# Optimization experiments

Measured on AMD Instinct MI355X. Metric: run time of the kernel, lower is better.

## Reference

```python
import jax, jax.numpy as jnp
import numpy as np

# Dims from init_kwargs
B, L, D = 32, 512, 1024
NSEC = 4
SSIZE = D // NSEC          # 256
LATENT = 256
N_TOKENS = 32
BANDS = ((0, 64), (16, 128), (32, 192), (64, 256))
COEF = 0.1


def _dct_mat(N):
    # torch_dct.dct (DCT-II, unnormalized, factor 2): X[k] = 2*sum_n x[n] cos(pi*k*(2n+1)/(2N))
    n = jnp.arange(N, dtype=jnp.float32)
    k = jnp.arange(N, dtype=jnp.float32)[:, None]
    return 2.0 * jnp.cos(jnp.pi * (2.0 * n + 1.0) * k / (2.0 * N))  # [k, n]


def _idct_mat(N):
    # exact inverse of the above (DCT-III form): x[n] = (1/N)*(X[0]/2 + sum_{k>=1} X[k] cos(pi*k*(2n+1)/(2N)))
    k = jnp.arange(N, dtype=jnp.float32)
    n = jnp.arange(N, dtype=jnp.float32)[:, None]
    M = jnp.cos(jnp.pi * k * (2.0 * n + 1.0) / (2.0 * N)) / N
    return M.at[:, 0].set(1.0 / (2.0 * N))  # [n, k]


def setup_inputs() -> dict:
    key = jax.random.key(0)
    k1, k2, k3 = jax.random.split(key, 3)
    encoding = jax.random.normal(k1, (B, L, D), dtype=jnp.float32)
    W = jax.random.normal(k2, (LATENT, SSIZE), dtype=jnp.float32) / np.float32(np.sqrt(SSIZE))
    b = jax.random.normal(k3, (LATENT,), dtype=jnp.float32) * 0.01
    return {"encoding": encoding, "W": W, "b": b}


def reference(encoding, W, b):
    # encoding: [B, L, D] -> [B, L, NSEC, SSIZE]
    enc = encoding.reshape(B, L, NSEC, SSIZE)
    # Literal semantics of the torch code: H = enc[:,:,i] is [B,L,S]; H.T -> [S,L,B];
    # dct/idct act over the LAST axis (= batch), scaling indexes the seq axis.
    C = _dct_mat(B)   # [k, b]
    M = _idct_mat(B)  # [b, k]
    # DCT along batch axis for all sectors at once: [k, L, NSEC, SSIZE]
    Dk = jnp.einsum('kb,blns->klns', C, enc)
    # Per-sector band scaling along the seq axis
    seq = jnp.arange(L)
    mask = jnp.stack(
        [jnp.where((seq < lo) | (seq >= hi), jnp.float32(COEF), jnp.float32(1.0)) for (lo, hi) in BANDS],
        axis=1,
    )  # [L, NSEC]
    Dk = Dk * mask[None, :, :, None]
    # IDCT back along batch axis: [B, L, NSEC, SSIZE]
    filt = jnp.einsum('bk,klns->blns', M, Dk)
    # Linear(SSIZE -> LATENT) + tanh, then keep first N_TOKENS positions
    y = jnp.tanh(jnp.einsum('blns,os->blno', filt, W) + b)
    return y[:, :N_TOKENS]
```

## Files before the change

kernel.cpp:

```cpp
#include <hip/hip_runtime.h>
#include <math.h>

#define LSEQ   512
#define DDIM   1024
#define KDIM   256
#define COLS   256
#define ROWS   4096
#define COEF   0.1f

#define TR     64
#define TC     64
#define BK     128


__device__ __forceinline__ float tanh_fast(float x) {
    return 1.0f - 2.0f / (__expf(2.0f * x) + 1.0f);
}

__global__ __launch_bounds__(256, 1)
void spectral_gemm_kernel(const float* __restrict__ enc,
                          const float* __restrict__ W,
                          const float* __restrict__ bias,
                          float* __restrict__ out) {
    __shared__ float4 As[TR * (BK / 4)];
    __shared__ float4 Ws[TC * (BK / 4)];

    const int t      = threadIdx.x;
    const int tile_r = blockIdx.x * TR;
    const int tile_c = blockIdx.y * TC;

    const float4* __restrict__ srcA =
        (const float4*)(enc + (size_t)(tile_r >> 7) * (size_t)(LSEQ * DDIM)
                            + (size_t)(tile_r & 127) * KDIM);
    const float4* __restrict__ srcW = (const float4*)(W + (size_t)tile_c * KDIM);

    const int tx = t & 15, ty = t >> 4;
    const int sA = ty & 7;
    const int sW = tx & 7;
    const int ra = ty * 4;
    const int ca = tx * 4;

    float acc[4][4] = {{0.f,0.f,0.f,0.f},{0.f,0.f,0.f,0.f},
                       {0.f,0.f,0.f,0.f},{0.f,0.f,0.f,0.f}};

    for (int p = 0; p < 2; ++p) {
        if (p) __syncthreads();

        #pragma unroll
        for (int i = 0; i < 8; ++i) {
            const int f    = t + i * 256;
            const int r    = f >> 5;
            const int k4   = f & 31;
            const int phys = k4 ^ ((r >> 2) & 7);
            As[r * 32 + phys] = srcA[r * 64 + 32 * p + k4];
            Ws[r * 32 + phys] = srcW[r * 64 + 32 * p + k4];
        }
        __syncthreads();

        #pragma unroll 8
        for (int k4 = 0; k4 < 32; ++k4) {
            const int pa = k4 ^ sA;
            const int pw = k4 ^ sW;
            float4 a[4], w[4];
            #pragma unroll
            for (int i = 0; i < 4; ++i) a[i] = As[(ra + i) * 32 + pa];
            #pragma unroll
            for (int j = 0; j < 4; ++j) w[j] = Ws[(ca + j) * 32 + pw];
            #pragma unroll
            for (int i = 0; i < 4; ++i)
                #pragma unroll
                for (int j = 0; j < 4; ++j) {
                    acc[i][j] += a[i].x * w[j].x;
                    acc[i][j] += a[i].y * w[j].y;
                    acc[i][j] += a[i].z * w[j].z;
                    acc[i][j] += a[i].w * w[j].w;
                }
        }
    }

    const float4 b4 = *(const float4*)&bias[tile_c + ca];
    #pragma unroll
    for (int i = 0; i < 4; ++i) {
        const int row = tile_r + ra + i;
        const int n = row & 3;
        const int l = (row >> 2) & 31;
        const float scale = (n == 0 || (n == 1 && l >= 16)) ? 1.0f : COEF;
        float4 o;
        o.x = tanh_fast(scale * acc[i][0] + b4.x);
        o.y = tanh_fast(scale * acc[i][1] + b4.y);
        o.z = tanh_fast(scale * acc[i][2] + b4.z);
        o.w = tanh_fast(scale * acc[i][3] + b4.w);
        *(float4*)&out[(size_t)row * COLS + tile_c + ca] = o;
    }
}

extern "C" void kernel_launch(void* const* d_in, const int* in_sizes, int n_in,
                              void* d_out, int out_size, void* d_ws, size_t ws_size,
                              hipStream_t stream) {
    const float* enc  = (const float*)d_in[0];
    const float* W    = (const float*)d_in[1];
    const float* bias = (const float*)d_in[2];
    float* out = (float*)d_out;

    dim3 grid(ROWS / TR, COLS / TC);
    spectral_gemm_kernel<<<grid, dim3(256), 0, stream>>>(enc, W, bias, out);
}
```

Measured before the change: 101.1 us.

## Use split-bf16 MFMA matrix cores for the projection GEMM

Replaces the FP32 FMA inner loop with bf16 MFMA 16x16x32 instructions, splitting each fp32 value into high and low bf16 parts and using three products to approximate fp32 accuracy. Row tile is halved to 32 so the grid gets more blocks, and launch bounds now allow two blocks per CU. The goal is to cut vector ALU time on a GEMM of 4096x256x256. In exchange, the split conversion in the load path adds VALU work, and the result carries a small precision loss compared with true fp32.

Result: faster. 93.72 us (-7.3%).

```diff
diff --git a/kernel.cpp b/kernel.cpp
--- a/kernel.cpp
+++ b/kernel.cpp
@@ -8,89 +8,127 @@
 #define ROWS   4096
 #define COEF   0.1f
 
-#define TR     64
+#define TR     32
 #define TC     64
 #define BK     128
+#define RSTR   128
 
+
+typedef __attribute__((ext_vector_type(8))) short short8;
+typedef __attribute__((ext_vector_type(4))) float float4v;
 
 __device__ __forceinline__ float tanh_fast(float x) {
     return 1.0f - 2.0f / (__expf(2.0f * x) + 1.0f);
 }
 
-__global__ __launch_bounds__(256, 1)
-void spectral_gemm_kernel(const float* __restrict__ enc,
+__device__ __forceinline__ void split_bf16(float x, unsigned short& h, unsigned short& l) {
+    union { float f; unsigned u; } a, hb, rb;
+    a.f = x;
+    const unsigned hu = (a.u + 0x7fffu + ((a.u >> 16) & 1u)) & 0xffff0000u;
+    h = (unsigned short)(hu >> 16);
+    hb.u = hu;
+    rb.f = x - hb.f;
+    l = (unsigned short)((rb.u + 0x7fffu + ((rb.u >> 16) & 1u)) >> 16);
+}
+
+__global__ __launch_bounds__(256, 2)
+void spectral_mfma_kernel(const float* __restrict__ enc,
                           const float* __restrict__ W,
                           const float* __restrict__ bias,
                           float* __restrict__ out) {
-    __shared__ float4 As[TR * (BK / 4)];
-    __shared__ float4 Ws[TC * (BK / 4)];
+    __shared__ short Ah[TR * RSTR], Al[TR * RSTR];
+    __shared__ short Wh[TC * RSTR], Wl[TC * RSTR];
 
     const int t      = threadIdx.x;
     const int tile_r = blockIdx.x * TR;
     const int tile_c = blockIdx.y * TC;
 
-    const float4* __restrict__ srcA =
-        (const float4*)(enc + (size_t)(tile_r >> 7) * (size_t)(LSEQ * DDIM)
-                            + (size_t)(tile_r & 127) * KDIM);
-    const float4* __restrict__ srcW = (const float4*)(W + (size_t)tile_c * KDIM);
+    const float* __restrict__ srcA = enc + (size_t)(tile_r >> 7) * (size_t)(LSEQ * DDIM)
+                                         + (size_t)(tile_r & 127) * KDIM;
+    const float* __restrict__ srcW = W + (size_t)tile_c * KDIM;
 
-    const int tx = t & 15, ty = t >> 4;
-    const int sA = ty & 7;
-    const int sW = tx & 7;
-    const int ra = ty * 4;
-    const int ca = tx * 4;
+    const int lane = t & 63;
+    const int wv   = t >> 6;
+    const int m0   = (wv & 1) * 16;
+    const int n0   = (wv >> 1) * 32;
+    const int fm   = lane & 15;
+    const int kq   = lane >> 4;
 
-    float acc[4][4] = {{0.f,0.f,0.f,0.f},{0.f,0.f,0.f,0.f},
-                       {0.f,0.f,0.f,0.f},{0.f,0.f,0.f,0.f}};
+    float4v acc0 = {0.f, 0.f, 0.f, 0.f};
+    float4v acc1 = {0.f, 0.f, 0.f, 0.f};
 
     for (int p = 0; p < 2; ++p) {
         if (p) __syncthreads();
 
         #pragma unroll
-        for (int i = 0; i < 8; ++i) {
-            const int f    = t + i * 256;
-            const int r    = f >> 5;
-            const int k4   = f & 31;
-            const int phys = k4 ^ ((r >> 2) & 7);
-            As[r * 32 + phys] = srcA[r * 64 + 32 * p + k4];
-            Ws[r * 32 + phys] = srcW[r * 64 + 32 * p + k4];
+        for (int i = 0; i < 2; ++i) {
+            const int q = t + i * 256;
+            const int r = q >> 4, s = q & 15;
+            const float* g = srcA + (size_t)r * KDIM + p * BK + s * 8;
+            const float4 x0 = *(const float4*)g;
+            const float4 x1 = *(const float4*)(g + 4);
+            const float xs[8] = {x0.x, x0.y, x0.z, x0.w, x1.x, x1.y, x1.z, x1.w};
+            unsigned short h[8], l[8];
+            #pragma unroll
+            for (int j = 0; j < 8; ++j) split_bf16(xs[j], h[j], l[j]);
+            const int phys = (s ^ (r & 15)) * 8;
+            short8 hv, lv;
+            #pragma unroll
+            for (int j = 0; j < 8; ++j) { hv[j] = (short)h[j]; lv[j] = (short)l[j]; }
+            *(short8*)&Ah[r * RSTR + phys] = hv;
+            *(short8*)&Al[r * RSTR + phys] = lv;
+        }
+        #pragma unroll
+        for (int i = 0; i < 4; ++i) {
+            const int q = t + i * 256;
+            const int r = q >> 4, s = q & 15;
+            const float* g = srcW + (size_t)r * KDIM + p * BK + s * 8;
+            const float4 x0 = *(const float4*)g;
+            const float4 x1 = *(const float4*)(g + 4);
+            const float xs[8] = {x0.x, x0.y, x0.z, x0.w, x1.x, x1.y, x1.z, x1.w};
+            unsigned short h[8], l[8];
+            #pragma unroll
+            for (int j = 0; j < 8; ++j) split_bf16(xs[j], h[j], l[j]);
+            const int phys = (s ^ (r & 15)) * 8;
+            short8 hv, lv;
+            #pragma unroll
+            for (int j = 0; j < 8; ++j) { hv[j] = (short)h[j]; lv[j] = (short)l[j]; }
+            *(short8*)&Wh[r * RSTR + phys] = hv;
+            *(short8*)&Wl[r * RSTR + phys] = lv;
         }
         __syncthreads();
 
-        #pragma unroll 8
-        for (int k4 = 0; k4 < 32; ++k4) {
-            const int pa = k4 ^ sA;
-            const int pw = k4 ^ sW;
-            float4 a[4], w[4];
-            #pragma unroll
-            for (int i = 0; i < 4; ++i) a[i] = As[(ra + i) * 32 + pa];
-            #pragma unroll
-            for (int j = 0; j < 4; ++j) w[j] = Ws[(ca + j) * 32 + pw];
-            #pragma unroll
-            for (int i = 0; i < 4; ++i)
-                #pragma unroll
-                for (int j = 0; j < 4; ++j) {
-                    acc[i][j] += a[i].x * w[j].x;
-                    acc[i][j] += a[i].y * w[j].y;
-                    acc[i][j] += a[i].z * w[j].z;
-                    acc[i][j] += a[i].w * w[j].w;
-                }
+        #pragma unroll
+        for (int ks = 0; ks < 4; ++ks) {
+            const int sb = ks * 4 + kq;
+            const int so = (sb ^ fm) * 8;
+            const short8 ah  = *(const short8*)&Ah[(m0 + fm) * RSTR + so];
+            const short8 al  = *(const short8*)&Al[(m0 + fm) * RSTR + so];
+            const short8 bh0 = *(const short8*)&Wh[(n0 + fm) * RSTR + so];
+            const short8 bl0 = *(const short8*)&Wl[(n0 + fm) * RSTR + so];
+            const short8 bh1 = *(const short8*)&Wh[(n0 + 16 + fm) * RSTR + so];
+            const short8 bl1 = *(const short8*)&Wl[(n0 + 16 + fm) * RSTR + so];
+            acc0 = __builtin_amdgcn_mfma_f32_16x16x32_bf16(ah, bh0, acc0, 0, 0, 0);
+            acc1 = __builtin_amdgcn_mfma_f32_16x16x32_bf16(ah, bh1, acc1, 0, 0, 0);
+            acc0 = __builtin_amdgcn_mfma_f32_16x16x32_bf16(ah, bl0, acc0, 0, 0, 0);
+            acc1 = __builtin_amdgcn_mfma_f32_16x16x32_bf16(ah, bl1, acc1, 0, 0, 0);
+            acc0 = __builtin_amdgcn_mfma_f32_16x16x32_bf16(al, bh0, acc0, 0, 0, 0);
+            acc1 = __builtin_amdgcn_mfma_f32_16x16x32_bf16(al, bh1, acc1, 0, 0, 0);
         }
     }
 
-    const float4 b4 = *(const float4*)&bias[tile_c + ca];
+    const int rbase = tile_r + m0 + kq * 4;
+    const int c0 = tile_c + n0 + fm;
+    const int c1 = c0 + 16;
+    const float b0 = bias[c0], b1 = bias[c1];
     #pragma unroll
-    for (int i = 0; i < 4; ++i) {
-        const int row = tile_r + ra + i;
-        const int n = row & 3;
-        const int l = (row >> 2) & 31;
-        const float scale = (n == 0 || (n == 1 && l >= 16)) ? 1.0f : COEF;
-        float4 o;
-        o.x = tanh_fast(scale * acc[i][0] + b4.x);
-        o.y = tanh_fast(scale * acc[i][1] + b4.y);
-        o.z = tanh_fast(scale * acc[i][2] + b4.z);
-        o.w = tanh_fast(scale * acc[i][3] + b4.w);
-        *(float4*)&out[(size_t)row * COLS + tile_c + ca] = o;
+    for (int reg = 0; reg < 4; ++reg) {
+        const int row = rbase + reg;
+        const int n  = row & 3;
+        const int li = (row >> 2) & 31;
+        const float scale = (n == 0 || (n == 1 && li >= 16)) ? 1.0f : COEF;
+        out[(size_t)row * COLS + c0] = tanh_fast(scale * acc0[reg] + b0);
+        out[(size_t)row * COLS + c1] = tanh_fast(scale * acc1[reg] + b1);
     }
 }
 
@@ -103,5 +141,5 @@
     float* out = (float*)d_out;
 
     dim3 grid(ROWS / TR, COLS / TC);
-    spectral_gemm_kernel<<<grid, dim3(256), 0, stream>>>(enc, W, bias, out);
+    spectral_mfma_kernel<<<grid, dim3(256), 0, stream>>>(enc, W, bias, out);
 }
```
